# Performance work log

Measured on AMD Instinct MI355X. Metric: run time of the kernel, lower is better.

The kernel has to match this reference:

```python
import jax, jax.numpy as jnp
import numpy as np

N_NODES = 100000
N_EDGES = 1600000
N_IN = 512
N_H = 64


def setup_inputs() -> dict:
    key = jax.random.key(0)
    ks = jax.random.split(key, 9)
    x_1 = jax.random.normal(ks[0], (1, N_NODES, N_IN), dtype=jnp.float32)
    x_2 = jax.random.normal(ks[1], (1, N_NODES, N_IN), dtype=jnp.float32)
    edge_row = jax.random.randint(ks[2], (N_EDGES,), 0, N_NODES, dtype=jnp.int32)
    edge_col = jax.random.randint(ks[3], (N_EDGES,), 0, N_NODES, dtype=jnp.int32)
    edge_weight = jax.random.uniform(ks[4], (N_EDGES,), dtype=jnp.float32)
    # GCN fc: Linear(n_in, n_h, bias=False), xavier_uniform init
    lim_fc = float(np.sqrt(6.0 / (N_IN + N_H)))
    fc_weight = jax.random.uniform(ks[5], (N_H, N_IN), minval=-lim_fc, maxval=lim_fc, dtype=jnp.float32)
    gcn_bias = jnp.zeros((N_H,), dtype=jnp.float32)
    prelu_a = jnp.array(0.25, dtype=jnp.float32)  # nn.PReLU default single weight
    lim_lin = float(np.sqrt(1.0 / N_H))  # torch Linear default init bound
    lin_weight = jax.random.uniform(ks[6], (N_H, N_H), minval=-lim_lin, maxval=lim_lin, dtype=jnp.float32)
    lin_bias = jax.random.uniform(ks[7], (N_H,), minval=-lim_lin, maxval=lim_lin, dtype=jnp.float32)
    return {
        "x_1": x_1, "x_2": x_2,
        "edge_row": edge_row, "edge_col": edge_col, "edge_weight": edge_weight,
        "fc_weight": fc_weight, "gcn_bias": gcn_bias, "prelu_a": prelu_a,
        "lin_weight": lin_weight, "lin_bias": lin_bias,
    }


def reference(x_1, x_2, edge_row, edge_col, edge_weight,
              fc_weight, gcn_bias, prelu_a, lin_weight, lin_bias):
    def gcn(x):
        # fc: [1,N,F] @ W^T -> [N, H]
        h = jnp.einsum('bnf,hf->bnh', x, fc_weight)[0]
        # spmm: out[r] += w * h[c]  (COO adjacency)
        msgs = edge_weight[:, None] * h[edge_col]            # [E, H]
        agg = jax.ops.segment_sum(msgs, edge_row, num_segments=N_NODES)
        out = agg + gcn_bias
        return jnp.where(out >= 0, out, prelu_a * out)       # PReLU, shape [N, H]

    h_1 = gcn(x_1)
    h_2 = gcn(x_2)
    z_1 = (h_1 @ lin_weight.T + lin_bias).sum(axis=1)        # [N]
    z_2 = (h_2 @ lin_weight.T + lin_bias).sum(axis=1)        # [N]
    return jnp.concatenate([z_1, z_2], axis=0)               # [2N]
```

## Files before the change

### kernel.cpp

```cpp
#include <hip/hip_runtime.h>

#define F_IN 512
#define HDIM 64
#define RSHIFT 7
#define RWIDTH 128
#define MAXNB 1024
#define CHUNK 4096

typedef _Float16 f16;
typedef _Float16 f16x2 __attribute__((ext_vector_type(2)));
typedef _Float16 f16x8 __attribute__((ext_vector_type(8)));
typedef float f32x4 __attribute__((ext_vector_type(4)));

__global__ void prep_kernel(const float* __restrict__ linW,
                            const float* __restrict__ linB,
                            float* __restrict__ wsum) {
    int k = threadIdx.x;
    float s = 0.f;
    for (int j = 0; j < HDIM; ++j) s += linW[j * HDIM + k];
    wsum[k] = s;
    if (k == 0) {
        float b = 0.f;
        for (int j = 0; j < HDIM; ++j) b += linB[j];
        wsum[HDIM] = b;
    }
}

__global__ __launch_bounds__(256) void prep_w16_kernel(const float* __restrict__ W,
                                                       f16* __restrict__ wf) {
    int t = blockIdx.x * 256 + threadIdx.x;
    int s = t >> 8;
    int c = (t >> 6) & 3;
    int l = t & 63;
    int row = c * 16 + (l & 15);
    int kb = s * 32 + ((l >> 4) << 3);
#pragma unroll
    for (int j = 0; j < 8; ++j)
        wf[(size_t)t * 8 + j] = (f16)W[row * F_IN + kb + j];
}

__global__ void zero_int_kernel(int* __restrict__ p, int n) {
    int i = blockIdx.x * blockDim.x + threadIdx.x;
    if (i < n) p[i] = 0;
}

__global__ __launch_bounds__(256) void bhist_kernel(const int* __restrict__ row,
                                                    int* __restrict__ bh,
                                                    int n_edges, int NB) {
    __shared__ int lh[MAXNB];
    for (int i = threadIdx.x; i < NB; i += 256) lh[i] = 0;
    __syncthreads();
    for (int e = blockIdx.x * 256 + threadIdx.x; e < n_edges; e += gridDim.x * 256)
        atomicAdd(&lh[row[e] >> RSHIFT], 1);
    __syncthreads();
    for (int i = threadIdx.x; i < NB; i += 256)
        if (lh[i]) atomicAdd(&bh[i], lh[i]);
}

__global__ __launch_bounds__(1024) void bscan_kernel(const int* __restrict__ bh,
                                                     int* __restrict__ boff,
                                                     int* __restrict__ gcur,
                                                     int* __restrict__ ptr,
                                                     int NB, int n_nodes, int n_edges) {
    __shared__ int s[1024];
    const int t = threadIdx.x;
    int v = (t < NB) ? bh[t] : 0;
    s[t] = v;
    __syncthreads();
#pragma unroll
    for (int off = 1; off < 1024; off <<= 1) {
        int x = (t >= off) ? s[t - off] : 0;
        __syncthreads();
        s[t] += x;
        __syncthreads();
    }
    if (t < NB) {
        int o = s[t] - v;
        boff[t] = o;
        gcur[t] = o;
    }
    if (t == NB) boff[NB] = n_edges;
    if (t == 0) ptr[n_nodes] = n_edges;
}

__global__ __launch_bounds__(256) void part_kernel(const int* __restrict__ row,
                                                   const int* __restrict__ col,
                                                   const float* __restrict__ w,
                                                   int* __restrict__ gcur,
                                                   int2* __restrict__ etmp,
                                                   int n_edges, int NB) {
    __shared__ int2 stg[CHUNK];
    __shared__ unsigned short sbin[CHUNK];
    __shared__ int lh[MAXNB];
    __shared__ int lofs[MAXNB];
    __shared__ int psum[256];
    const int t = threadIdx.x;
    const int base = blockIdx.x * CHUNK;
    const int cnt = min(CHUNK, n_edges - base);

    for (int i = t; i < NB; i += 256) lh[i] = 0;
    __syncthreads();
    for (int i = t; i < cnt; i += 256)
        atomicAdd(&lh[row[base + i] >> RSHIFT], 1);
    __syncthreads();
    int loc[4];
    int s0 = 0;
#pragma unroll
    for (int j = 0; j < 4; ++j) {
        int b = t * 4 + j;
        int c = (b < NB) ? lh[b] : 0;
        loc[j] = s0;
        s0 += c;
    }
    psum[t] = s0;
    __syncthreads();
#pragma unroll
    for (int off = 1; off < 256; off <<= 1) {
        int x = (t >= off) ? psum[t - off] : 0;
        __syncthreads();
        psum[t] += x;
        __syncthreads();
    }
    int pbase = psum[t] - s0;
#pragma unroll
    for (int j = 0; j < 4; ++j) {
        int b = t * 4 + j;
        if (b < NB) lofs[b] = pbase + loc[j];
    }
    __syncthreads();
    for (int i = t; i < cnt; i += 256) {
        int r = row[base + i];
        int b = r >> RSHIFT;
        int p = atomicAdd(&lofs[b], 1);
        stg[p] = make_int2(__float_as_int(w[base + i]),
                           (col[base + i] << RSHIFT) | (r & (RWIDTH - 1)));
        sbin[p] = (unsigned short)b;
    }
    __syncthreads();
    for (int b = t; b < NB; b += 256) {
        int c = lh[b];
        if (c) {
            int lstart = lofs[b] - c;
            int gb = atomicAdd(&gcur[b], c);
            lh[b] = gb - lstart;
        }
    }
    __syncthreads();
    for (int p = t; p < cnt; p += 256) {
        int b = sbin[p];
        etmp[lh[b] + p] = stg[p];
    }
}

__global__ __launch_bounds__(256) void bsort_kernel(const int* __restrict__ boff,
                                                    const int2* __restrict__ etmp,
                                                    int2* __restrict__ ebin,
                                                    int* __restrict__ ptr,
                                                    int n_nodes) {
    __shared__ int nh[RWIDTH], lo[RWIDTH], lc[RWIDTH];
    const int b = blockIdx.x;
    const int t = threadIdx.x;
    const int e0 = boff[b], e1 = boff[b + 1];
    const int cnt = e1 - e0;
    if (t < RWIDTH) nh[t] = 0;
    __syncthreads();
    for (int i = t; i < cnt; i += 256)
        atomicAdd(&nh[etmp[e0 + i].y & (RWIDTH - 1)], 1);
    __syncthreads();
    if (t < RWIDTH) lo[t] = nh[t];
    __syncthreads();
    for (int off = 1; off < RWIDTH; off <<= 1) {
        int x = 0;
        if (t < RWIDTH && t >= off) x = lo[t - off];
        __syncthreads();
        if (t < RWIDTH) lo[t] += x;
        __syncthreads();
    }
    if (t < RWIDTH) {
        int ex = lo[t] - nh[t];
        lc[t] = ex;
        int node = b * RWIDTH + t;
        if (node < n_nodes) ptr[node] = e0 + ex;
    }
    __syncthreads();
    for (int i = t; i < cnt; i += 256) {
        int2 r = etmp[e0 + i];
        int p = atomicAdd(&lc[r.y & (RWIDTH - 1)], 1);
        ebin[e0 + p] = make_int2(r.x, r.y >> RSHIFT);
    }
}

__global__ __launch_bounds__(256) void gemm_both_kernel(const float* __restrict__ X1,
                                                        const float* __restrict__ X2,
                                                        const f16* __restrict__ wf,
                                                        f16* __restrict__ H,
                                                        int n_nodes) {
    const float* X = blockIdx.y ? X2 : X1;
    const int pass = blockIdx.y;
    const int lane = threadIdx.x & 63;
    const int w = threadIdx.x >> 6;
    const int m0 = blockIdx.x * 64 + w * 16;
    int arow = m0 + (lane & 15);
    if (arow >= n_nodes) arow = n_nodes - 1;
    const float* xp = X + (size_t)arow * F_IN + ((lane >> 4) << 3);
    const f16x8* wfv = reinterpret_cast<const f16x8*>(wf);

    f32x4 acc0 = {}, acc1 = {}, acc2 = {}, acc3 = {};
    for (int s = 0; s < 16; ++s) {
        const f16x8* bp = wfv + (size_t)(s * 4) * 64 + lane;
        f16x8 b0 = bp[0];
        f16x8 b1 = bp[64];
        f16x8 b2 = bp[128];
        f16x8 b3 = bp[192];
        float4 xa = *reinterpret_cast<const float4*>(xp + s * 32);
        float4 xb = *reinterpret_cast<const float4*>(xp + s * 32 + 4);
        f16x8 a;
        a[0] = (f16)xa.x; a[1] = (f16)xa.y; a[2] = (f16)xa.z; a[3] = (f16)xa.w;
        a[4] = (f16)xb.x; a[5] = (f16)xb.y; a[6] = (f16)xb.z; a[7] = (f16)xb.w;
        acc0 = __builtin_amdgcn_mfma_f32_16x16x32_f16(a, b0, acc0, 0, 0, 0);
        acc1 = __builtin_amdgcn_mfma_f32_16x16x32_f16(a, b1, acc1, 0, 0, 0);
        acc2 = __builtin_amdgcn_mfma_f32_16x16x32_f16(a, b2, acc2, 0, 0, 0);
        acc3 = __builtin_amdgcn_mfma_f32_16x16x32_f16(a, b3, acc3, 0, 0, 0);
    }

    const int colj = lane & 15;
#pragma unroll
    for (int j = 0; j < 4; ++j) {
        int r = m0 + ((lane >> 4) << 2) + j;
        if (r < n_nodes) {
            f16* hp = H + (size_t)r * 2 * HDIM + colj * 2 + pass;
            hp[0]  = (f16)acc0[j];
            hp[32] = (f16)acc1[j];
            hp[64] = (f16)acc2[j];
            hp[96] = (f16)acc3[j];
        }
    }
}

__global__ __launch_bounds__(256) void agg_both_kernel(const int* __restrict__ ptr,
                                                       const int2* __restrict__ ebin,
                                                       const f16* __restrict__ h,
                                                       const float* __restrict__ gbias,
                                                       const float* __restrict__ wsum,
                                                       const float* __restrict__ prelu_a,
                                                       float* __restrict__ z,
                                                       int n_nodes) {
    const int lane = threadIdx.x & 63;
    const int wv = threadIdx.x >> 6;
    const int n = blockIdx.x * 4 + wv;
    if (n >= n_nodes) return;
    const f16x2* hv = reinterpret_cast<const f16x2*>(h) + lane;
    const int p0 = __builtin_amdgcn_readfirstlane(ptr[n]);
    const int p1 = __builtin_amdgcn_readfirstlane(ptr[n + 1]);
    float acc1 = 0.f, acc2 = 0.f;
    int i = p0;
    for (; i + 3 < p1; i += 4) {
        int2 e0 = ebin[i];
        int2 e1 = ebin[i + 1];
        int2 e2 = ebin[i + 2];
        int2 e3 = ebin[i + 3];
        f16x2 h0 = hv[(size_t)e0.y * HDIM];
        f16x2 h1 = hv[(size_t)e1.y * HDIM];
        f16x2 h2 = hv[(size_t)e2.y * HDIM];
        f16x2 h3 = hv[(size_t)e3.y * HDIM];
        float w0 = __int_as_float(e0.x), w1 = __int_as_float(e1.x);
        float w2 = __int_as_float(e2.x), w3 = __int_as_float(e3.x);
        acc1 = fmaf(w0, (float)h0[0], acc1);
        acc2 = fmaf(w0, (float)h0[1], acc2);
        acc1 = fmaf(w1, (float)h1[0], acc1);
        acc2 = fmaf(w1, (float)h1[1], acc2);
        acc1 = fmaf(w2, (float)h2[0], acc1);
        acc2 = fmaf(w2, (float)h2[1], acc2);
        acc1 = fmaf(w3, (float)h3[0], acc1);
        acc2 = fmaf(w3, (float)h3[1], acc2);
    }
    for (; i < p1; ++i) {
        int2 e0 = ebin[i];
        f16x2 h0 = hv[(size_t)e0.y * HDIM];
        float w0 = __int_as_float(e0.x);
        acc1 = fmaf(w0, (float)h0[0], acc1);
        acc2 = fmaf(w0, (float)h0[1], acc2);
    }
    const float a = prelu_a[0];
    const float gb = gbias[lane];
    const float wl = wsum[lane];
    float v1 = acc1 + gb;
    float v2 = acc2 + gb;
    v1 = (v1 >= 0.f) ? v1 : a * v1;
    v2 = (v2 >= 0.f) ? v2 : a * v2;
    float q1 = v1 * wl;
    float q2 = v2 * wl;
#pragma unroll
    for (int m = 32; m >= 1; m >>= 1) {
        q1 += __shfl_xor(q1, m, 64);
        q2 += __shfl_xor(q2, m, 64);
    }
    if (lane == 0) {
        z[n] = q1 + wsum[HDIM];
        z[n + n_nodes] = q2 + wsum[HDIM];
    }
}

extern "C" void kernel_launch(void* const* d_in, const int* in_sizes, int n_in,
                              void* d_out, int out_size, void* d_ws, size_t ws_size,
                              hipStream_t stream) {
    const float* x1    = (const float*)d_in[0];
    const float* x2    = (const float*)d_in[1];
    const int*   erow  = (const int*)d_in[2];
    const int*   ecol  = (const int*)d_in[3];
    const float* ew    = (const float*)d_in[4];
    const float* fcw   = (const float*)d_in[5];
    const float* gbias = (const float*)d_in[6];
    const float* pa    = (const float*)d_in[7];
    const float* linw  = (const float*)d_in[8];
    const float* linb  = (const float*)d_in[9];
    float* out = (float*)d_out;

    const int n_nodes = in_sizes[0] / F_IN;
    const int n_edges = in_sizes[2];
    const int NB = (n_nodes + RWIDTH - 1) >> RSHIFT;

    f16*   h16  = (f16*)d_ws;
    f16*   wf   = h16 + (size_t)n_nodes * 2 * HDIM;
    int2*  etmp = (int2*)(wf + 64 * F_IN);
    int2*  ebin = etmp + n_edges;
    int*   bh   = (int*)(ebin + n_edges);
    int*   boff = bh + MAXNB;
    int*   gcur = boff + MAXNB + 1;
    int*   ptr  = gcur + MAXNB;
    float* wsum = (float*)(ptr + n_nodes + 1);

    prep_kernel<<<1, 64, 0, stream>>>(linw, linb, wsum);
    prep_w16_kernel<<<16, 256, 0, stream>>>(fcw, wf);

    zero_int_kernel<<<(NB + 255) / 256, 256, 0, stream>>>(bh, NB);
    bhist_kernel<<<256, 256, 0, stream>>>(erow, bh, n_edges, NB);
    bscan_kernel<<<1, 1024, 0, stream>>>(bh, boff, gcur, ptr, NB, n_nodes, n_edges);
    part_kernel<<<(n_edges + CHUNK - 1) / CHUNK, 256, 0, stream>>>(erow, ecol, ew, gcur,
                                                                   etmp, n_edges, NB);
    bsort_kernel<<<NB, 256, 0, stream>>>(boff, etmp, ebin, ptr, n_nodes);

    const int gemm_grid = (n_nodes + 63) / 64;
    const int fin_grid  = (n_nodes + 3) / 4;
    gemm_both_kernel<<<dim3(gemm_grid, 2), 256, 0, stream>>>(x1, x2, wf, h16, n_nodes);
    agg_both_kernel<<<fin_grid, 256, 0, stream>>>(ptr, ebin, h16, gbias, wsum, pa,
                                                  out, n_nodes);
}
```

Measured before the change: 249.7 us.

## Stage X tiles into LDS via direct global-to-LDS loads with XOR swizzle

```diff
diff --git a/kernel.cpp b/kernel.cpp
--- a/kernel.cpp
+++ b/kernel.cpp
@@ -6,11 +6,16 @@
 #define RWIDTH 128
 #define MAXNB 1024
 #define CHUNK 4096
+#define BKF 128
 
 typedef _Float16 f16;
 typedef _Float16 f16x2 __attribute__((ext_vector_type(2)));
 typedef _Float16 f16x8 __attribute__((ext_vector_type(8)));
 typedef float f32x4 __attribute__((ext_vector_type(4)));
+
+#define GLOAD_LDS16(src, dst)                                                        \
+    __builtin_amdgcn_global_load_lds((const __attribute__((address_space(1))) void*)(src), \
+                                     (__attribute__((address_space(3))) void*)(dst), 16, 0, 0)
 
 __global__ void prep_kernel(const float* __restrict__ linW,
                             const float* __restrict__ linB,
@@ -195,38 +200,65 @@
                                                         const f16* __restrict__ wf,
                                                         f16* __restrict__ H,
                                                         int n_nodes) {
+    __shared__ float xs[64 * BKF];
     const float* X = blockIdx.y ? X2 : X1;
     const int pass = blockIdx.y;
-    const int lane = threadIdx.x & 63;
-    const int w = threadIdx.x >> 6;
-    const int m0 = blockIdx.x * 64 + w * 16;
-    int arow = m0 + (lane & 15);
-    if (arow >= n_nodes) arow = n_nodes - 1;
-    const float* xp = X + (size_t)arow * F_IN + ((lane >> 4) << 3);
+    const int t = threadIdx.x;
+    const int lane = t & 63;
+    const int w = t >> 6;
+    const int m0 = blockIdx.x * 64;
     const f16x8* wfv = reinterpret_cast<const f16x8*>(wf);
 
+    const int srow_base = w * 2 + (lane >> 5);
+    const int ssub = (lane & 31) << 4;
+    char* sdst_base = (char*)xs + w * 1024;
+
+    const int rl = w * 16 + (lane & 15);
+    const int g = lane >> 4;
+    const int sw = (rl & 7) << 4;
+    const char* xrow = (const char*)xs + rl * 512;
+
     f32x4 acc0 = {}, acc1 = {}, acc2 = {}, acc3 = {};
-    for (int s = 0; s < 16; ++s) {
-        const f16x8* bp = wfv + (size_t)(s * 4) * 64 + lane;
-        f16x8 b0 = bp[0];
-        f16x8 b1 = bp[64];
-        f16x8 b2 = bp[128];
-        f16x8 b3 = bp[192];
-        float4 xa = *reinterpret_cast<const float4*>(xp + s * 32);
-        float4 xb = *reinterpret_cast<const float4*>(xp + s * 32 + 4);
-        f16x8 a;
-        a[0] = (f16)xa.x; a[1] = (f16)xa.y; a[2] = (f16)xa.z; a[3] = (f16)xa.w;
-        a[4] = (f16)xb.x; a[5] = (f16)xb.y; a[6] = (f16)xb.z; a[7] = (f16)xb.w;
-        acc0 = __builtin_amdgcn_mfma_f32_16x16x32_f16(a, b0, acc0, 0, 0, 0);
-        acc1 = __builtin_amdgcn_mfma_f32_16x16x32_f16(a, b1, acc1, 0, 0, 0);
-        acc2 = __builtin_amdgcn_mfma_f32_16x16x32_f16(a, b2, acc2, 0, 0, 0);
-        acc3 = __builtin_amdgcn_mfma_f32_16x16x32_f16(a, b3, acc3, 0, 0, 0);
-    }
-
+
+    for (int c = 0; c < 4; ++c) {
+        const int k0 = c * BKF;
+#pragma unroll
+        for (int p = 0; p < 8; ++p) {
+            int row = p * 8 + srow_base;
+            int gm = m0 + row;
+            if (gm >= n_nodes) gm = n_nodes - 1;
+            const char* src = (const char*)(X + (size_t)gm * F_IN + k0) +
+                              (ssub ^ ((row & 7) << 4));
+            GLOAD_LDS16(src, sdst_base + p * 4096);
+        }
+        __syncthreads();
+#pragma unroll
+        for (int ks = 0; ks < 4; ++ks) {
+            const int s = c * 4 + ks;
+            const f16x8* bp = wfv + (size_t)(s * 4) * 64 + lane;
+            f16x8 b0 = bp[0];
+            f16x8 b1 = bp[64];
+            f16x8 b2 = bp[128];
+            f16x8 b3 = bp[192];
+            const int c0 = ks * 128 + g * 32;
+            float4 xa = *reinterpret_cast<const float4*>(xrow + (c0 ^ sw));
+            float4 xb = *reinterpret_cast<const float4*>(xrow + ((c0 + 16) ^ sw));
+            f16x8 a;
+            a[0] = (f16)xa.x; a[1] = (f16)xa.y; a[2] = (f16)xa.z; a[3] = (f16)xa.w;
+            a[4] = (f16)xb.x; a[5] = (f16)xb.y; a[6] = (f16)xb.z; a[7] = (f16)xb.w;
+            acc0 = __builtin_amdgcn_mfma_f32_16x16x32_f16(a, b0, acc0, 0, 0, 0);
+            acc1 = __builtin_amdgcn_mfma_f32_16x16x32_f16(a, b1, acc1, 0, 0, 0);
+            acc2 = __builtin_amdgcn_mfma_f32_16x16x32_f16(a, b2, acc2, 0, 0, 0);
+            acc3 = __builtin_amdgcn_mfma_f32_16x16x32_f16(a, b3, acc3, 0, 0, 0);
+        }
+        __syncthreads();
+    }
+
+    const int m0w = m0 + w * 16;
     const int colj = lane & 15;
 #pragma unroll
     for (int j = 0; j < 4; ++j) {
-        int r = m0 + ((lane >> 4) << 2) + j;
+        int r = m0w + ((lane >> 4) << 2) + j;
         if (r < n_nodes) {
             f16* hp = H + (size_t)r * 2 * HDIM + colj * 2 + pass;
             hp[0]  = (f16)acc0[j];
```

Result: faster. 229.8 us (-8.0%).

## Double-buffer X tiles in LDS via direct global-to-LDS loads and fuse both inputs

Applied to the files above, without the earlier changes.

```diff
diff --git a/kernel.cpp b/kernel.cpp
--- a/kernel.cpp
+++ b/kernel.cpp
@@ -6,11 +6,16 @@
 #define RWIDTH 128
 #define MAXNB 1024
 #define CHUNK 4096
+#define BK 32
 
 typedef _Float16 f16;
 typedef _Float16 f16x2 __attribute__((ext_vector_type(2)));
 typedef _Float16 f16x8 __attribute__((ext_vector_type(8)));
 typedef float f32x4 __attribute__((ext_vector_type(4)));
+
+#define GLOAD_LDS16(src, dst)                                                        \
+    __builtin_amdgcn_global_load_lds((const __attribute__((address_space(1))) void*)(src), \
+                                     (__attribute__((address_space(3))) void*)(dst), 16, 0, 0)
 
 __global__ void prep_kernel(const float* __restrict__ linW,
                             const float* __restrict__ linB,
@@ -190,49 +195,102 @@
     }
 }
 
-__global__ __launch_bounds__(256) void gemm_both_kernel(const float* __restrict__ X1,
-                                                        const float* __restrict__ X2,
-                                                        const f16* __restrict__ wf,
-                                                        f16* __restrict__ H,
-                                                        int n_nodes) {
-    const float* X = blockIdx.y ? X2 : X1;
-    const int pass = blockIdx.y;
-    const int lane = threadIdx.x & 63;
-    const int w = threadIdx.x >> 6;
-    const int m0 = blockIdx.x * 64 + w * 16;
-    int arow = m0 + (lane & 15);
-    if (arow >= n_nodes) arow = n_nodes - 1;
-    const float* xp = X + (size_t)arow * F_IN + ((lane >> 4) << 3);
+__global__ __launch_bounds__(256, 4) void gemm_both_kernel(const float* __restrict__ X1,
+                                                           const float* __restrict__ X2,
+                                                           const f16* __restrict__ wf,
+                                                           f16* __restrict__ H,
+                                                           int n_nodes) {
+    __shared__ float4 xs_v[2048];
+    char* xs = (char*)xs_v;
+    const int t = threadIdx.x;
+    const int l = t & 63;
+    const int w = t >> 6;
+    const int m0 = blockIdx.x * 64;
     const f16x8* wfv = reinterpret_cast<const f16x8*>(wf);
 
-    f32x4 acc0 = {}, acc1 = {}, acc2 = {}, acc3 = {};
-    for (int s = 0; s < 16; ++s) {
-        const f16x8* bp = wfv + (size_t)(s * 4) * 64 + lane;
+    const int srow_off = l >> 3;
+    const int sswz = (((l & 7) ^ (l >> 3)) << 4);
+
+#define STAGE(c, buf)                                                                   \
+    {                                                                                   \
+        _Pragma("unroll")                                                               \
+        for (int p = 0; p < 4; ++p) {                                                   \
+            int row = ((p & 1) << 5) + (w << 3) + srow_off;                             \
+            int gm = m0 + row;                                                          \
+            if (gm >= n_nodes) gm = n_nodes - 1;                                        \
+            const float* Xp = (p >> 1) ? X2 : X1;                                       \
+            const char* src = (const char*)(Xp + (size_t)gm * F_IN + (c) * BK) + sswz;  \
+            GLOAD_LDS16(src, xs + (buf) * 16384 + p * 4096 + w * 1024);                 \
+        }                                                                               \
+    }
+
+    const int rl = w * 16 + (l & 15);
+    const int g = l >> 4;
+    const int swz = (rl & 7) << 4;
+
+    f32x4 a00 = {}, a01 = {}, a02 = {}, a03 = {};
+    f32x4 a10 = {}, a11 = {}, a12 = {}, a13 = {};
+
+    STAGE(0, 0)
+    __syncthreads();
+    int buf = 0;
+#pragma unroll 2
+    for (int c = 0; c < 16; ++c) {
+        if (c < 15) STAGE(c + 1, buf ^ 1)
+        const f16x8* bp = wfv + (size_t)(c * 4) * 64 + l;
         f16x8 b0 = bp[0];
         f16x8 b1 = bp[64];
         f16x8 b2 = bp[128];
         f16x8 b3 = bp[192];
-        float4 xa = *reinterpret_cast<const float4*>(xp + s * 32);
-        float4 xb = *reinterpret_cast<const float4*>(xp + s * 32 + 4);
-        f16x8 a;
-        a[0] = (f16)xa.x; a[1] = (f16)xa.y; a[2] = (f16)xa.z; a[3] = (f16)xa.w;
-        a[4] = (f16)xb.x; a[5] = (f16)xb.y; a[6] = (f16)xb.z; a[7] = (f16)xb.w;
-        acc0 = __builtin_amdgcn_mfma_f32_16x16x32_f16(a, b0, acc0, 0, 0, 0);
-        acc1 = __builtin_amdgcn_mfma_f32_16x16x32_f16(a, b1, acc1, 0, 0, 0);
-        acc2 = __builtin_amdgcn_mfma_f32_16x16x32_f16(a, b2, acc2, 0, 0, 0);
-        acc3 = __builtin_amdgcn_mfma_f32_16x16x32_f16(a, b3, acc3, 0, 0, 0);
-    }
-
-    const int colj = lane & 15;
-#pragma unroll
-    for (int j = 0; j < 4; ++j) {
-        int r = m0 + ((lane >> 4) << 2) + j;
-        if (r < n_nodes) {
-            f16* hp = H + (size_t)r * 2 * HDIM + colj * 2 + pass;
-            hp[0]  = (f16)acc0[j];
-            hp[32] = (f16)acc1[j];
-            hp[64] = (f16)acc2[j];
-            hp[96] = (f16)acc3[j];
+        const char* base = xs + buf * 16384 + rl * 128;
+#pragma unroll
+        for (int pass = 0; pass < 2; ++pass) {
+            float4 xa = *reinterpret_cast<const float4*>(base + pass * 8192 + ((g * 32) ^ swz));
+            float4 xb = *reinterpret_cast<const float4*>(base + pass * 8192 + ((g * 32 + 16) ^ swz));
+            f16x8 a;
+            a[0] = (f16)xa.x; a[1] = (f16)xa.y; a[2] = (f16)xa.z; a[3] = (f16)xa.w;
+            a[4] = (f16)xb.x; a[5] = (f16)xb.y; a[6] = (f16)xb.z; a[7] = (f16)xb.w;
+            if (pass == 0) {
+                a00 = __builtin_amdgcn_mfma_f32_16x16x32_f16(a, b0, a00, 0, 0, 0);
+                a01 = __builtin_amdgcn_mfma_f32_16x16x32_f16(a, b1, a01, 0, 0, 0);
+                a02 = __builtin_amdgcn_mfma_f32_16x16x32_f16(a, b2, a02, 0, 0, 0);
+                a03 = __builtin_amdgcn_mfma_f32_16x16x32_f16(a, b3, a03, 0, 0, 0);
+            } else {
+                a10 = __builtin_amdgcn_mfma_f32_16x16x32_f16(a, b0, a10, 0, 0, 0);
+                a11 = __builtin_amdgcn_mfma_f32_16x16x32_f16(a, b1, a11, 0, 0, 0);
+                a12 = __builtin_amdgcn_mfma_f32_16x16x32_f16(a, b2, a12, 0, 0, 0);
+                a13 = __builtin_amdgcn_mfma_f32_16x16x32_f16(a, b3, a13, 0, 0, 0);
+            }
+        }
+        __syncthreads();
+        buf ^= 1;
+    }
+#undef STAGE
+
+    {
+        f16* tile = (f16*)xs;
+        const int colj = l & 15;
+        const int rbase = w * 16 + g * 4;
+#pragma unroll
+        for (int j = 0; j < 4; ++j) {
+            f16* tp = tile + (rbase + j) * 128 + colj * 2;
+            tp[0]  = (f16)a00[j];
+            tp[1]  = (f16)a10[j];
+            tp[32] = (f16)a01[j];
+            tp[33] = (f16)a11[j];
+            tp[64] = (f16)a02[j];
+            tp[65] = (f16)a12[j];
+            tp[96] = (f16)a03[j];
+            tp[97] = (f16)a13[j];
+        }
+        __syncthreads();
+        const int row = t >> 2;
+        const int gm = m0 + row;
+        if (gm < n_nodes) {
+            const float4* sp = reinterpret_cast<const float4*>(xs + row * 256 + (t & 3) * 64);
+            float4* dp = reinterpret_cast<float4*>((char*)H + (size_t)gm * 256 + (t & 3) * 64);
+#pragma unroll
+            for (int q = 0; q < 4; ++q) dp[q] = sp[q];
         }
     }
 }
@@ -342,7 +400,7 @@
 
     const int gemm_grid = (n_nodes + 63) / 64;
     const int fin_grid  = (n_nodes + 3) / 4;
-    gemm_both_kernel<<<dim3(gemm_grid, 2), 256, 0, stream>>>(x1, x2, wf, h16, n_nodes);
+    gemm_both_kernel<<<gemm_grid, 256, 0, stream>>>(x1, x2, wf, h16, n_nodes);
     agg_both_kernel<<<fin_grid, 256, 0, stream>>>(ptr, ebin, h16, gbias, wsum, pa,
                                                   out, n_nodes);
 }
```

Result: faster. 234.4 us (-6.1%).

## Pipeline GEMM loads through LDS with async global-to-LDS copies, fuse both inputs

Applied to the files above, without the earlier changes.

```diff
diff --git a/kernel.cpp b/kernel.cpp
--- a/kernel.cpp
+++ b/kernel.cpp
@@ -11,6 +11,10 @@
 typedef _Float16 f16x2 __attribute__((ext_vector_type(2)));
 typedef _Float16 f16x8 __attribute__((ext_vector_type(8)));
 typedef float f32x4 __attribute__((ext_vector_type(4)));
+
+#define GLOAD_LDS16(src, dst)                                                        \
+    __builtin_amdgcn_global_load_lds((const __attribute__((address_space(1))) void*)(src), \
+                                     (__attribute__((address_space(3))) void*)(dst), 16, 0, 0)
 
 __global__ void prep_kernel(const float* __restrict__ linW,
                             const float* __restrict__ linB,
@@ -195,44 +199,98 @@
                                                         const f16* __restrict__ wf,
                                                         f16* __restrict__ H,
                                                         int n_nodes) {
-    const float* X = blockIdx.y ? X2 : X1;
-    const int pass = blockIdx.y;
-    const int lane = threadIdx.x & 63;
-    const int w = threadIdx.x >> 6;
-    const int m0 = blockIdx.x * 64 + w * 16;
-    int arow = m0 + (lane & 15);
-    if (arow >= n_nodes) arow = n_nodes - 1;
-    const float* xp = X + (size_t)arow * F_IN + ((lane >> 4) << 3);
-    const f16x8* wfv = reinterpret_cast<const f16x8*>(wf);
-
-    f32x4 acc0 = {}, acc1 = {}, acc2 = {}, acc3 = {};
-    for (int s = 0; s < 16; ++s) {
-        const f16x8* bp = wfv + (size_t)(s * 4) * 64 + lane;
-        f16x8 b0 = bp[0];
-        f16x8 b1 = bp[64];
-        f16x8 b2 = bp[128];
-        f16x8 b3 = bp[192];
-        float4 xa = *reinterpret_cast<const float4*>(xp + s * 32);
-        float4 xb = *reinterpret_cast<const float4*>(xp + s * 32 + 4);
-        f16x8 a;
-        a[0] = (f16)xa.x; a[1] = (f16)xa.y; a[2] = (f16)xa.z; a[3] = (f16)xa.w;
-        a[4] = (f16)xb.x; a[5] = (f16)xb.y; a[6] = (f16)xb.z; a[7] = (f16)xb.w;
-        acc0 = __builtin_amdgcn_mfma_f32_16x16x32_f16(a, b0, acc0, 0, 0, 0);
-        acc1 = __builtin_amdgcn_mfma_f32_16x16x32_f16(a, b1, acc1, 0, 0, 0);
-        acc2 = __builtin_amdgcn_mfma_f32_16x16x32_f16(a, b2, acc2, 0, 0, 0);
-        acc3 = __builtin_amdgcn_mfma_f32_16x16x32_f16(a, b3, acc3, 0, 0, 0);
-    }
-
-    const int colj = lane & 15;
-#pragma unroll
-    for (int j = 0; j < 4; ++j) {
-        int r = m0 + ((lane >> 4) << 2) + j;
-        if (r < n_nodes) {
-            f16* hp = H + (size_t)r * 2 * HDIM + colj * 2 + pass;
-            hp[0]  = (f16)acc0[j];
-            hp[32] = (f16)acc1[j];
-            hp[64] = (f16)acc2[j];
-            hp[96] = (f16)acc3[j];
+    __shared__ char xs[81920];
+    const int t = threadIdx.x;
+    const int l = t & 63;
+    const int w = t >> 6;
+    const int m0 = blockIdx.x * 64;
+    int srow = m0 + l;
+    if (srow >= n_nodes) srow = n_nodes - 1;
+    const char* sx1 = (const char*)(X1 + (size_t)srow * F_IN) + (w << 5);
+    const char* sx2 = (const char*)(X2 + (size_t)srow * F_IN) + (w << 5);
+    const char* wfb = (const char*)wf;
+    const int g = l >> 4;
+    const int rl16 = (w * 16 + (l & 15)) * 16;
+
+    f32x4 p00 = {}, p01 = {}, p02 = {}, p03 = {};
+    f32x4 p10 = {}, p11 = {}, p12 = {}, p13 = {};
+
+#define STAGE(c)                                                                  \
+    {                                                                             \
+        char* bb = xs + ((c) & 3) * 20480;                                        \
+        GLOAD_LDS16(sx1 + (c) * 128,      bb + w * 2048);                         \
+        GLOAD_LDS16(sx1 + (c) * 128 + 16, bb + w * 2048 + 1024);                  \
+        GLOAD_LDS16(sx2 + (c) * 128,      bb + 8192 + w * 2048);                  \
+        GLOAD_LDS16(sx2 + (c) * 128 + 16, bb + 8192 + w * 2048 + 1024);           \
+        GLOAD_LDS16(wfb + (c) * 4096 + w * 1024 + l * 16, bb + 16384 + w * 1024); \
+    }
+
+#define COMPUTE(c)                                                                \
+    {                                                                             \
+        const char* bb = xs + ((c) & 3) * 20480;                                  \
+        f16x8 B0 = *(const f16x8*)(bb + 16384 + l * 16);                          \
+        f16x8 B1 = *(const f16x8*)(bb + 16384 + 1024 + l * 16);                   \
+        f16x8 B2 = *(const f16x8*)(bb + 16384 + 2048 + l * 16);                   \
+        f16x8 B3 = *(const f16x8*)(bb + 16384 + 3072 + l * 16);                   \
+        float4 xa = *(const float4*)(bb + g * 2048 + rl16);                       \
+        float4 xb = *(const float4*)(bb + g * 2048 + 1024 + rl16);                \
+        f16x8 a;                                                                  \
+        a[0] = (f16)xa.x; a[1] = (f16)xa.y; a[2] = (f16)xa.z; a[3] = (f16)xa.w;   \
+        a[4] = (f16)xb.x; a[5] = (f16)xb.y; a[6] = (f16)xb.z; a[7] = (f16)xb.w;   \
+        p00 = __builtin_amdgcn_mfma_f32_16x16x32_f16(a, B0, p00, 0, 0, 0);        \
+        p01 = __builtin_amdgcn_mfma_f32_16x16x32_f16(a, B1, p01, 0, 0, 0);        \
+        p02 = __builtin_amdgcn_mfma_f32_16x16x32_f16(a, B2, p02, 0, 0, 0);        \
+        p03 = __builtin_amdgcn_mfma_f32_16x16x32_f16(a, B3, p03, 0, 0, 0);        \
+        float4 ya = *(const float4*)(bb + 8192 + g * 2048 + rl16);                \
+        float4 yb = *(const float4*)(bb + 8192 + g * 2048 + 1024 + rl16);         \
+        a[0] = (f16)ya.x; a[1] = (f16)ya.y; a[2] = (f16)ya.z; a[3] = (f16)ya.w;   \
+        a[4] = (f16)yb.x; a[5] = (f16)yb.y; a[6] = (f16)yb.z; a[7] = (f16)yb.w;   \
+        p10 = __builtin_amdgcn_mfma_f32_16x16x32_f16(a, B0, p10, 0, 0, 0);        \
+        p11 = __builtin_amdgcn_mfma_f32_16x16x32_f16(a, B1, p11, 0, 0, 0);        \
+        p12 = __builtin_amdgcn_mfma_f32_16x16x32_f16(a, B2, p12, 0, 0, 0);        \
+        p13 = __builtin_amdgcn_mfma_f32_16x16x32_f16(a, B3, p13, 0, 0, 0);        \
+    }
+
+#define ITER(c, WN)                                         \
+    asm volatile("s_waitcnt vmcnt(" WN ")" ::: "memory");   \
+    __builtin_amdgcn_s_barrier();                           \
+    if ((c) + 3 < 16) STAGE((c) + 3)                        \
+    COMPUTE(c)
+
+    STAGE(0) STAGE(1) STAGE(2)
+    ITER(0, "10")  ITER(1, "10")  ITER(2, "10")  ITER(3, "10")
+    ITER(4, "10")  ITER(5, "10")  ITER(6, "10")  ITER(7, "10")
+    ITER(8, "10")  ITER(9, "10")  ITER(10, "10") ITER(11, "10")
+    ITER(12, "10") ITER(13, "10") ITER(14, "5")  ITER(15, "0")
+#undef ITER
+#undef COMPUTE
+#undef STAGE
+
+    __syncthreads();
+    {
+        f16* tile = (f16*)xs;
+        const int colj = l & 15;
+        const int rbase = w * 16 + g * 4;
+#pragma unroll
+        for (int j = 0; j < 4; ++j) {
+            f16* tp = tile + (rbase + j) * 128 + colj * 2;
+            tp[0]  = (f16)p00[j];
+            tp[1]  = (f16)p10[j];
+            tp[32] = (f16)p01[j];
+            tp[33] = (f16)p11[j];
+            tp[64] = (f16)p02[j];
+            tp[65] = (f16)p12[j];
+            tp[96] = (f16)p03[j];
+            tp[97] = (f16)p13[j];
+        }
+        __syncthreads();
+        const int row = t >> 2;
+        const int gm = m0 + row;
+        if (gm < n_nodes) {
+            const float4* sp = reinterpret_cast<const float4*>(xs + row * 256 + (t & 3) * 64);
+            float4* dp = reinterpret_cast<float4*>((char*)H + (size_t)gm * 256 + (t & 3) * 64);
+#pragma unroll
+            for (int q = 0; q < 4; ++q) dp[q] = sp[q];
         }
     }
 }
@@ -342,7 +400,7 @@
 
     const int gemm_grid = (n_nodes + 63) / 64;
     const int fin_grid  = (n_nodes + 3) / 4;
-    gemm_both_kernel<<<dim3(gemm_grid, 2), 256, 0, stream>>>(x1, x2, wf, h16, n_nodes);
+    gemm_both_kernel<<<gemm_grid, 256, 0, stream>>>(x1, x2, wf, h16, n_nodes);
     agg_both_kernel<<<fin_grid, 256, 0, stream>>>(ptr, ebin, h16, gbias, wsum, pa,
                                                   out, n_nodes);
 }
```

New measurement: 251.7 us. No clear change (+0.8%).
